# Optimization experiments

Measured on AMD Instinct MI355X. Metric: run time of the kernel, lower is better.

Reference implementation:

```python
import jax, jax.numpy as jnp
import numpy as np

B, L, E, H, D = 2, 2048, 2048, 16, 128
EPS = 1e-6


def _rms(x, scale):
    # RMSNorm over head_dim, computed in float32 (matches torch RMSNorm)
    x32 = x.astype(jnp.float32)
    n = jnp.mean(x32 * x32, axis=-1, keepdims=True)
    return (scale.astype(jnp.float32) * (x32 * jax.lax.rsqrt(n + EPS))).astype(x.dtype)


def _rotary(x, rope):
    # x: [B, L, H, D]; rope: [B, L, D//2, 2]
    xs = x.astype(jnp.float32).reshape(*x.shape[:-1], -1, 2)  # [B,L,H,D/2,2]
    rc = rope.reshape(xs.shape[0], xs.shape[1], 1, xs.shape[3], 2).astype(jnp.float32)
    out = jnp.stack(
        [xs[..., 0] * rc[..., 0] - xs[..., 1] * rc[..., 1],
         xs[..., 1] * rc[..., 0] + xs[..., 0] * rc[..., 1]], -1)
    return out.reshape(x.shape).astype(x.dtype)


def setup_inputs() -> dict:
    key = jax.random.key(0)
    ks = jax.random.split(key, 9)
    s = 0.02  # weight init scale (~kaiming fan_in for E=2048)
    return {
        "inputs_q": jax.random.normal(ks[0], (B, L, E), jnp.float32),
        "inputs_kv": jax.random.normal(ks[1], (B, L, E), jnp.float32),
        "bias": jax.random.normal(ks[2], (B, 1, L, L), jnp.float32),
        "rope_q": jax.random.normal(ks[3], (B, L, D // 2, 2), jnp.float32),
        "rope_k": jax.random.normal(ks[4], (B, L, D // 2, 2), jnp.float32),
        "Wq": jax.random.normal(ks[5], (E, E), jnp.float32) * s,
        "Wk": jax.random.normal(ks[6], (E, E), jnp.float32) * s,
        "Wv": jax.random.normal(ks[7], (E, E), jnp.float32) * s,
        "Wo": jax.random.normal(ks[8], (E, E), jnp.float32) * s,
        "q_scale": jnp.ones((D,), jnp.float32),
        "k_scale": jnp.ones((D,), jnp.float32),
    }


def reference(inputs_q, inputs_kv, bias, rope_q, rope_k, Wq, Wk, Wv, Wo, q_scale, k_scale):
    Bq, Lq, _ = inputs_q.shape
    Lk = inputs_kv.shape[1]
    dtype = inputs_q.dtype
    # QKV projections (torch Linear: y = x @ W.T)
    q = (inputs_q @ Wq.T).reshape(Bq, Lq, H, D)
    k = (inputs_kv @ Wk.T).reshape(Bq, Lk, H, D)
    v = (inputs_kv @ Wv.T).reshape(Bq, Lk, H, D)
    # qk_norm
    q = _rms(q, q_scale)
    k = _rms(k, k_scale)
    # rotary embeddings
    q = _rotary(q, rope_q)
    k = _rotary(k, rope_k)
    # float32_logits
    q = q.astype(jnp.float32)
    k = k.astype(jnp.float32)
    # faithful to torch source: query.div_(depth ** (-0.5)) == q * sqrt(D)
    q = q / (D ** (-0.5))
    logits = jnp.einsum('bqhd,bkhd->bhqk', q, k) + bias.astype(jnp.float32)
    probs = jax.nn.softmax(logits, axis=-1).astype(dtype)
    # dropout_rate = 0.0 -> identity
    x = jnp.einsum('bhqk,bkhd->bqhd', probs, v).reshape(Bq, Lq, E)
    return x @ Wo.T
```

## Files before the change

### kernel.cpp

```cpp
#include <hip/hip_runtime.h>

#define Bb 2
#define Ll 2048
#define Ee 2048
#define Hh 16
#define Dd 128
#define BL (Bb * Ll)
#define NT (Ll / 64)
#define LOSCALE 1024.0f
#define INV_LOSCALE (1.0f / 1024.0f)
#define LOG2E 1.442695041f

typedef float f32x4 __attribute__((ext_vector_type(4)));
typedef _Float16 f16x8 __attribute__((ext_vector_type(8)));

__device__ __forceinline__ void gld_lds16(const void* g, void* l) {
  __builtin_amdgcn_global_load_lds((const __attribute__((address_space(1))) void*)g,
                                   (__attribute__((address_space(3))) void*)l, 16, 0, 0);
}

__device__ __forceinline__ float exp2_hw(float x) {
  float r;
  asm("v_exp_f32 %0, %1" : "=v"(r) : "v"(x));
  return r;
}

__global__ __launch_bounds__(256) void cvt_f32_f16(const float* __restrict__ in,
                                                   _Float16* __restrict__ out, int n4) {
  int i = blockIdx.x * 256 + threadIdx.x;
  if (i < n4) {
    float4 f = ((const float4*)in)[i];
    _Float16 o[4] = {(_Float16)f.x, (_Float16)f.y, (_Float16)f.z, (_Float16)f.w};
    ((uint2*)out)[i] = *(uint2*)o;
  }
}

__global__ __launch_bounds__(256) void cvt_split(const float* __restrict__ in,
                                                 _Float16* __restrict__ hi,
                                                 _Float16* __restrict__ lo, int n4) {
  int i = blockIdx.x * 256 + threadIdx.x;
  if (i < n4) {
    float4 f = ((const float4*)in)[i];
    float fa[4] = {f.x, f.y, f.z, f.w};
    _Float16 h[4], l[4];
    for (int j = 0; j < 4; ++j) {
      h[j] = (_Float16)fa[j];
      l[j] = (_Float16)((fa[j] - (float)h[j]) * LOSCALE);
    }
    ((uint2*)hi)[i] = *(uint2*)h;
    ((uint2*)lo)[i] = *(uint2*)l;
  }
}

__global__ __launch_bounds__(256) void bias_perm(const float* __restrict__ bias,
                                                 _Float16* __restrict__ out) {
  __shared__ float T[128][68];
  const int kt = blockIdx.x, qt = blockIdx.y, b = blockIdx.z;
  const float* src = bias + ((size_t)b * Ll + qt * 128) * Ll + kt * 64;
  const int t = threadIdx.x;
  for (int c = 0; c < 8; ++c) {
    int idx = c * 256 + t;
    int r = idx >> 4, col4 = (idx & 15) * 4;
    float4 v = *(const float4*)&src[(size_t)r * Ll + col4];
    T[r][col4 + 0] = v.x; T[r][col4 + 1] = v.y;
    T[r][col4 + 2] = v.z; T[r][col4 + 3] = v.w;
  }
  __syncthreads();
  _Float16* dst = out + ((((size_t)(b * 8 + (qt >> 1)) * NT + kt) * 16 + (qt & 1) * 8) * 64) * 16;
  for (int s = 0; s < 2; ++s) {
    int slot = t + s * 256;
    int w = slot >> 6, lane = slot & 63;
    int quad = lane >> 4, l16 = lane & 15;
    _Float16 vals[16];
    for (int nt = 0; nt < 4; ++nt)
      for (int r = 0; r < 4; ++r)
        vals[nt * 4 + r] = (_Float16)(T[w * 16 + quad * 4 + r][nt * 16 + l16] * LOG2E);
    *(uint4*)&dst[((size_t)w * 64 + lane) * 16] = *(uint4*)&vals[0];
    *(uint4*)&dst[((size_t)w * 64 + lane) * 16 + 8] = *(uint4*)&vals[8];
  }
}

template <typename OutT>
__global__ __launch_bounds__(256, 2) void gemm_bt(const _Float16* __restrict__ A,
                                                  const _Float16* __restrict__ Bw,
                                                  OutT* __restrict__ C, int M, int N, int K) {
  __shared__ _Float16 As[128 * 64];
  __shared__ _Float16 Bs[128 * 64];
  const int tid = threadIdx.x;
  const int wave = tid >> 6, lane = tid & 63;
  const int quad = lane >> 4, l16 = lane & 15;
  const int lrow = lane >> 3, lch = lane & 7;
  const int scol = (lch ^ lrow) * 8;
  const int bm = blockIdx.y * 128, bn = blockIdx.x * 128;
  const int wm = (wave >> 1) * 64, wn = (wave & 1) * 64;

  f32x4 acc[4][4] = {};

  for (int k0 = 0; k0 < K; k0 += 64) {
    for (int i = 0; i < 4; ++i) {
      int br = wave * 32 + i * 8;
      gld_lds16(&A[(size_t)(bm + br + lrow) * K + k0 + scol], &As[br * 64]);
      gld_lds16(&Bw[(size_t)(bn + br + lrow) * K + k0 + scol], &Bs[br * 64]);
    }
    __syncthreads();
    for (int ks = 0; ks < 2; ++ks) {
      f16x8 af[4], bf[4];
      for (int mt = 0; mt < 4; ++mt)
        af[mt] = *(const f16x8*)&As[(wm + mt * 16 + l16) * 64 +
                                    (((ks * 4 + quad) ^ (l16 & 7)) * 8)];
      for (int nt = 0; nt < 4; ++nt)
        bf[nt] = *(const f16x8*)&Bs[(wn + nt * 16 + l16) * 64 +
                                    (((ks * 4 + quad) ^ (l16 & 7)) * 8)];
      for (int mt = 0; mt < 4; ++mt)
        for (int nt = 0; nt < 4; ++nt)
          acc[mt][nt] = __builtin_amdgcn_mfma_f32_16x16x32_f16(af[mt], bf[nt], acc[mt][nt], 0, 0, 0);
    }
    __syncthreads();
  }

  for (int mt = 0; mt < 4; ++mt)
    for (int nt = 0; nt < 4; ++nt)
      for (int r = 0; r < 4; ++r) {
        int m = bm + wm + mt * 16 + quad * 4 + r;
        int n = bn + wn + nt * 16 + l16;
        C[(size_t)m * N + n] = (OutT)acc[mt][nt][r];
      }
}

__global__ __launch_bounds__(256, 2) void gemm_bt_split(
    const _Float16* __restrict__ Ah, const _Float16* __restrict__ Al,
    const _Float16* __restrict__ Bh, const _Float16* __restrict__ Bl,
    float* __restrict__ C, int M, int N, int K) {
  __shared__ _Float16 Ash[128 * 64];
  __shared__ _Float16 Asl[128 * 64];
  __shared__ _Float16 Bsh[128 * 64];
  __shared__ _Float16 Bsl[128 * 64];
  const int tid = threadIdx.x;
  const int wave = tid >> 6, lane = tid & 63;
  const int quad = lane >> 4, l16 = lane & 15;
  const int lrow = lane >> 3, lch = lane & 7;
  const int scol = (lch ^ lrow) * 8;
  const int bm = blockIdx.y * 128, bn = blockIdx.x * 128;
  const int wm = (wave >> 1) * 64, wn = (wave & 1) * 64;

  f32x4 acc_hh[4][4] = {};
  f32x4 acc_cr[4][4] = {};

  for (int k0 = 0; k0 < K; k0 += 64) {
    for (int i = 0; i < 4; ++i) {
      int br = wave * 32 + i * 8;
      size_t ga = (size_t)(bm + br + lrow) * K + k0 + scol;
      size_t gb = (size_t)(bn + br + lrow) * K + k0 + scol;
      gld_lds16(&Ah[ga], &Ash[br * 64]);
      gld_lds16(&Al[ga], &Asl[br * 64]);
      gld_lds16(&Bh[gb], &Bsh[br * 64]);
      gld_lds16(&Bl[gb], &Bsl[br * 64]);
    }
    __syncthreads();
    for (int ks = 0; ks < 2; ++ks) {
      const int sw = ((ks * 4 + quad) ^ (l16 & 7)) * 8;
      f16x8 afh[4], afl[4], bfh[4], bfl[4];
      for (int mt = 0; mt < 4; ++mt) {
        afh[mt] = *(const f16x8*)&Ash[(wm + mt * 16 + l16) * 64 + sw];
        afl[mt] = *(const f16x8*)&Asl[(wm + mt * 16 + l16) * 64 + sw];
      }
      for (int nt = 0; nt < 4; ++nt) {
        bfh[nt] = *(const f16x8*)&Bsh[(wn + nt * 16 + l16) * 64 + sw];
        bfl[nt] = *(const f16x8*)&Bsl[(wn + nt * 16 + l16) * 64 + sw];
      }
      for (int mt = 0; mt < 4; ++mt)
        for (int nt = 0; nt < 4; ++nt) {
          acc_hh[mt][nt] = __builtin_amdgcn_mfma_f32_16x16x32_f16(afh[mt], bfh[nt], acc_hh[mt][nt], 0, 0, 0);
          acc_cr[mt][nt] = __builtin_amdgcn_mfma_f32_16x16x32_f16(afh[mt], bfl[nt], acc_cr[mt][nt], 0, 0, 0);
          acc_cr[mt][nt] = __builtin_amdgcn_mfma_f32_16x16x32_f16(afl[mt], bfh[nt], acc_cr[mt][nt], 0, 0, 0);
        }
    }
    __syncthreads();
  }

  for (int mt = 0; mt < 4; ++mt)
    for (int nt = 0; nt < 4; ++nt)
      for (int r = 0; r < 4; ++r) {
        int m = bm + wm + mt * 16 + quad * 4 + r;
        int n = bn + wn + nt * 16 + l16;
        C[(size_t)m * N + n] = acc_hh[mt][nt][r] + acc_cr[mt][nt][r] * INV_LOSCALE;
      }
}

__global__ __launch_bounds__(256) void transpose_v(const _Float16* __restrict__ V,
                                                   _Float16* __restrict__ Vt) {
  __shared__ _Float16 T[64][72];
  const int bl0 = blockIdx.x * 64, n0 = blockIdx.y * 64;
  const int tid = threadIdx.x;
  for (int c = 0; c < 2; ++c) {
    int chunk = tid + c * 256;
    int r = chunk >> 3, cc = (chunk & 7) * 8;
    *(uint4*)&T[r][cc] = *(const uint4*)&V[(size_t)(bl0 + r) * Ee + n0 + cc];
  }
  __syncthreads();
  const int b = bl0 >> 11;
  const int k0 = bl0 & (Ll - 1);
  for (int c = 0; c < 2; ++c) {
    int chunk = tid + c * 256;
    int nr = chunk >> 3, kc = (chunk & 7) * 8;
    _Float16 tmp[8];
    for (int j = 0; j < 8; ++j) tmp[j] = T[kc + j][nr];
    *(uint4*)&Vt[((size_t)b * Ee + n0 + nr) * Ll + k0 + kc] = *(uint4*)tmp;
  }
}

__global__ __launch_bounds__(256) void rmsrope(const float* __restrict__ raw,
                                               const float* __restrict__ scale,
                                               const float* __restrict__ rope,
                                               _Float16* __restrict__ outh,
                                               _Float16* __restrict__ outl, float outmul) {
  int row = blockIdx.x * 4 + (threadIdx.x >> 6);
  int t = threadIdx.x & 63;
  float2 x = *(const float2*)&raw[(size_t)row * Dd + 2 * t];
  float ss = x.x * x.x + x.y * x.y;
  for (int off = 1; off < 64; off <<= 1) ss += __shfl_xor(ss, off);
  float inv = rsqrtf(ss * (1.0f / Dd) + 1e-6f);
  float2 sc = *(const float2*)&scale[2 * t];
  float y0 = x.x * inv * sc.x;
  float y1 = x.y * inv * sc.y;
  int bl = row >> 4;
  float2 cs = *(const float2*)&rope[(size_t)bl * Dd + 2 * t];
  float r0 = (y0 * cs.x - y1 * cs.y) * outmul;
  float r1 = (y1 * cs.x + y0 * cs.y) * outmul;
  _Float16 h[2] = {(_Float16)r0, (_Float16)r1};
  _Float16 l[2] = {(_Float16)(r0 - (float)h[0]), (_Float16)(r1 - (float)h[1])};
  *(uint*)&outh[(size_t)row * Dd + 2 * t] = *(uint*)h;
  *(uint*)&outl[(size_t)row * Dd + 2 * t] = *(uint*)l;
}

__global__ __launch_bounds__(512, 2) void attn(const _Float16* __restrict__ Qh_,
                                               const _Float16* __restrict__ Ql_,
                                               const _Float16* __restrict__ Kh_,
                                               const _Float16* __restrict__ Kl_,
                                               const _Float16* __restrict__ Vt_g,
                                               const _Float16* __restrict__ biasp,
                                               _Float16* __restrict__ O) {
  __shared__ _Float16 Ksh[64 * 128];
  __shared__ _Float16 Ksl[64 * 128];
  __shared__ _Float16 Vts[2][128 * 64];
  __shared__ _Float16 Ps[128 * 64];

  const int tid = threadIdx.x;
  const int wave = tid >> 6, lane = tid & 63;
  const int quad = lane >> 4, l16 = lane & 15;
  const int lrow8 = lane >> 3, lch8 = lane & 7;
  const int lrow16 = lane >> 4, lch16 = lane & 15;
  const int h = blockIdx.x;
  const int qt = blockIdx.y, q0 = qt * 128;
  const int b = blockIdx.z;

  f16x8 aqh[4], aql[4];
  {
    size_t qrow = (((size_t)b * Ll + q0 + wave * 16 + l16) * Hh + h) * Dd;
    for (int ks = 0; ks < 4; ++ks) {
      aqh[ks] = *(const f16x8*)&Qh_[qrow + ks * 32 + quad * 8];
      aql[ks] = *(const f16x8*)&Ql_[qrow + ks * 32 + quad * 8];
    }
  }
  const _Float16* Vbase = Vt_g + ((size_t)b * Ee + h * Dd) * Ll;
  const _Float16* bias_base = biasp + (size_t)(b * 8 + (qt >> 1)) * (NT * 16 * 1024) +
                              (size_t)((qt & 1) * 8 + wave) * 1024 + (size_t)lane * 16;

  f32x4 o_acc[8] = {};
  float m_r[4], l_r[4];
  for (int r = 0; r < 4; ++r) { m_r[r] = -1e30f; l_r[r] = 0.f; }

  auto stageK = [&](int kt) {
    const int k0 = kt * 64;
    for (int i = 0; i < 2; ++i) {
      int br = wave * 8 + i * 4;
      int row = br + lrow16;
      int sc = (lch16 ^ (row & 7)) * 8;
      size_t g = (((size_t)b * Ll + k0 + row) * Hh + h) * Dd + sc;
      gld_lds16(&Kh_[g], &Ksh[br * 128]);
      gld_lds16(&Kl_[g], &Ksl[br * 128]);
    }
  };
  auto stageV = [&](int nb, int kt) {
    const int k0 = kt * 64;
    for (int i = 0; i < 2; ++i) {
      int br = wave * 16 + i * 8;
      int row = br + lrow8;
      int sc = (lch8 ^ (row & 7)) * 8;
      gld_lds16(&Vbase[(size_t)row * Ll + k0 + sc], &Vts[nb][br * 64]);
    }
  };

  stageK(0);
  stageV(0, 0);
  __syncthreads();

  for (int kt = 0; kt < NT; ++kt) {
    const int cur = kt & 1;

    f16x8 bf0 = *(const f16x8*)&bias_base[(size_t)kt * 16384];
    f16x8 bf1 = *(const f16x8*)&bias_base[(size_t)kt * 16384 + 8];

    __builtin_amdgcn_s_setprio(1);
    f32x4 s[4] = {};
    for (int ks = 0; ks < 4; ++ks) {
      const int sw = ((ks * 4 + quad) ^ (l16 & 7)) * 8;
      for (int nt = 0; nt < 4; ++nt) {
        f16x8 bkh = *(const f16x8*)&Ksh[(nt * 16 + l16) * 128 + sw];
        f16x8 bkl = *(const f16x8*)&Ksl[(nt * 16 + l16) * 128 + sw];
        s[nt] = __builtin_amdgcn_mfma_f32_16x16x32_f16(aqh[ks], bkh, s[nt], 0, 0, 0);
        s[nt] = __builtin_amdgcn_mfma_f32_16x16x32_f16(aql[ks], bkh, s[nt], 0, 0, 0);
        s[nt] = __builtin_amdgcn_mfma_f32_16x16x32_f16(aqh[ks], bkl, s[nt], 0, 0, 0);
      }
    }
    __builtin_amdgcn_s_setprio(0);

    __syncthreads();

    if (kt + 1 < NT) {
      stageK(kt + 1);
      stageV(cur ^ 1, kt + 1);
    }

#pragma unroll
    for (int nt = 0; nt < 4; ++nt)
#pragma unroll
      for (int r = 0; r < 4; ++r) {
        float bv = (nt < 2) ? (float)bf0[nt * 4 + r] : (float)bf1[nt * 4 + r - 8];
        s[nt][r] += bv;
      }

    bool grow = false;
#pragma unroll
    for (int r = 0; r < 4; ++r) {
      float v = fmaxf(fmaxf(s[0][r], s[1][r]), fmaxf(s[2][r], s[3][r]));
      grow = grow || (v > m_r[r] + 8.f);
    }
    if (__any(grow)) {
#pragma unroll
      for (int r = 0; r < 4; ++r) {
        float v = fmaxf(fmaxf(s[0][r], s[1][r]), fmaxf(s[2][r], s[3][r]));
        for (int off = 1; off < 16; off <<= 1) v = fmaxf(v, __shfl_xor(v, off));
        float mn = fmaxf(m_r[r], v);
        float alpha = exp2_hw(m_r[r] - mn);
        m_r[r] = mn;
        l_r[r] *= alpha;
        for (int ot = 0; ot < 8; ++ot) o_acc[ot][r] *= alpha;
      }
    }
#pragma unroll
    for (int r = 0; r < 4; ++r) {
      int row = wave * 16 + quad * 4 + r;
      float sum = 0.f;
#pragma unroll
      for (int nt = 0; nt < 4; ++nt) {
        float p = exp2_hw(s[nt][r] - m_r[r]);
        sum += p;
        int col = nt * 16 + l16;
        Ps[row * 64 + (col ^ (((row >> 2) & 3) << 4))] = (_Float16)p;
      }
      l_r[r] += sum;
    }

    __builtin_amdgcn_s_setprio(1);
    for (int ks = 0; ks < 2; ++ks) {
      const int sw = ((ks * 4 + quad) ^ (l16 & 7)) * 8;
      int prow = wave * 16 + l16;
      f16x8 ap = *(const f16x8*)&Ps[prow * 64 +
                                    ((ks * 32 + quad * 8) ^ (((l16 >> 2) & 3) << 4))];
      for (int ot = 0; ot < 8; ++ot) {
        f16x8 bv = *(const f16x8*)&Vts[cur][(ot * 16 + l16) * 64 + sw];
        o_acc[ot] = __builtin_amdgcn_mfma_f32_16x16x32_f16(ap, bv, o_acc[ot], 0, 0, 0);
      }
    }
    __builtin_amdgcn_s_setprio(0);

    __syncthreads();
  }

  for (int r = 0; r < 4; ++r) {
    float l = l_r[r];
    for (int off = 1; off < 16; off <<= 1) l += __shfl_xor(l, off);
    l_r[r] = 1.f / l;
  }

  for (int ot = 0; ot < 8; ++ot)
    for (int r = 0; r < 4; ++r) {
      int mm = q0 + wave * 16 + quad * 4 + r;
      O[(((size_t)b * Ll + mm) * Hh + h) * Dd + ot * 16 + l16] =
          (_Float16)(o_acc[ot][r] * l_r[r]);
    }
}

extern "C" void kernel_launch(void* const* d_in, const int* in_sizes, int n_in,
                              void* d_out, int out_size, void* d_ws, size_t ws_size,
                              hipStream_t stream) {
  const float* inputs_q  = (const float*)d_in[0];
  const float* inputs_kv = (const float*)d_in[1];
  const float* bias      = (const float*)d_in[2];
  const float* rope_q    = (const float*)d_in[3];
  const float* rope_k    = (const float*)d_in[4];
  const float* Wq        = (const float*)d_in[5];
  const float* Wk        = (const float*)d_in[6];
  const float* Wv        = (const float*)d_in[7];
  const float* Wo        = (const float*)d_in[8];
  const float* q_scale   = (const float*)d_in[9];
  const float* k_scale   = (const float*)d_in[10];
  float* out = (float*)d_out;

  char* ws = (char*)d_ws;
  size_t o = 0;
  auto alloc = [&](size_t bytes) {
    char* p = ws + o;
    o += (bytes + 255) & ~(size_t)255;
    return p;
  };
  const size_t szX16 = (size_t)BL * Ee * 2;
  const size_t szW16 = (size_t)Ee * Ee * 2;
  _Float16* Xq_hi  = (_Float16*)alloc(szX16);
  _Float16* Xq_lo  = (_Float16*)alloc(szX16);
  _Float16* Xkv_hi = (_Float16*)alloc(szX16);
  _Float16* Xkv_lo = (_Float16*)alloc(szX16);
  _Float16* Wq_hi  = (_Float16*)alloc(szW16);
  _Float16* Wq_lo  = (_Float16*)alloc(szW16);
  _Float16* Wk_hi  = (_Float16*)alloc(szW16);
  _Float16* Wk_lo  = (_Float16*)alloc(szW16);
  _Float16* Wv_hi  = (_Float16*)alloc(szW16);
  _Float16* Wo_hi  = (_Float16*)alloc(szW16);
  float* Qraw = (float*)alloc((size_t)BL * Ee * 4);
  float* Kraw = (float*)alloc((size_t)BL * Ee * 4);
  _Float16* V16 = (_Float16*)alloc(szX16);
  _Float16* Q16h   = Xq_hi;
  _Float16* Q16l   = Xq_lo;
  _Float16* K16h   = Xkv_hi;
  _Float16* K16l   = Xkv_lo;
  _Float16* X16    = (_Float16*)Qraw;
  _Float16* Vt_g   = Wq_hi;
  _Float16* biasp  = (_Float16*)Kraw;

  const int nX4 = BL * Ee / 4;
  const int nW4 = Ee * Ee / 4;
  cvt_split<<<nX4 / 256, 256, 0, stream>>>(inputs_q, Xq_hi, Xq_lo, nX4);
  cvt_split<<<nX4 / 256, 256, 0, stream>>>(inputs_kv, Xkv_hi, Xkv_lo, nX4);
  cvt_split<<<nW4 / 256, 256, 0, stream>>>(Wq, Wq_hi, Wq_lo, nW4);
  cvt_split<<<nW4 / 256, 256, 0, stream>>>(Wk, Wk_hi, Wk_lo, nW4);
  cvt_f32_f16<<<nW4 / 256, 256, 0, stream>>>(Wv, Wv_hi, nW4);
  cvt_f32_f16<<<nW4 / 256, 256, 0, stream>>>(Wo, Wo_hi, nW4);

  dim3 gblk(Ee / 128, BL / 128);
  gemm_bt_split<<<gblk, 256, 0, stream>>>(Xq_hi, Xq_lo, Wq_hi, Wq_lo, Qraw, BL, Ee, Ee);
  gemm_bt_split<<<gblk, 256, 0, stream>>>(Xkv_hi, Xkv_lo, Wk_hi, Wk_lo, Kraw, BL, Ee, Ee);
  gemm_bt<_Float16><<<gblk, 256, 0, stream>>>(Xkv_hi, Wv_hi, V16, BL, Ee, Ee);

  transpose_v<<<dim3(BL / 64, Ee / 64), 256, 0, stream>>>(V16, Vt_g);

  rmsrope<<<BL * Hh / 4, 256, 0, stream>>>(Qraw, q_scale, rope_q, Q16h, Q16l,
                                           sqrtf((float)Dd) * LOG2E);
  rmsrope<<<BL * Hh / 4, 256, 0, stream>>>(Kraw, k_scale, rope_k, K16h, K16l, 1.0f);

  bias_perm<<<dim3(NT, Ll / 128, Bb), 256, 0, stream>>>(bias, biasp);

  attn<<<dim3(Hh, Ll / 128, Bb), 512, 0, stream>>>(Q16h, Q16l, K16h, K16l, Vt_g, biasp, X16);

  gemm_bt<float><<<gblk, 256, 0, stream>>>(X16, Wo_hi, out, BL, Ee, Ee);
}
```

Baseline: 700.4 us.

## Double-buffer K tiles and enlarge attention blocks to 256 query rows

Grows each attention workgroup from 8 to 16 waves, so each block covers 256 query rows and every K/V tile loaded into LDS is shared by twice as many rows. K is now double-buffered like V, and the prefetch of the next tile is issued before the QK MFMAs, which removes one barrier per iteration. The bias indexing is adjusted to match the new tiling. The cost is a 1024-thread block with higher LDS use (K double buffer plus a larger P buffer), which may lower occupancy and halves the number of blocks in the grid.

```diff
diff --git a/kernel.cpp b/kernel.cpp
--- a/kernel.cpp
+++ b/kernel.cpp
@@ -233,17 +233,17 @@
   *(uint*)&outl[(size_t)row * Dd + 2 * t] = *(uint*)l;
 }
 
-__global__ __launch_bounds__(512, 2) void attn(const _Float16* __restrict__ Qh_,
-                                               const _Float16* __restrict__ Ql_,
-                                               const _Float16* __restrict__ Kh_,
-                                               const _Float16* __restrict__ Kl_,
-                                               const _Float16* __restrict__ Vt_g,
-                                               const _Float16* __restrict__ biasp,
-                                               _Float16* __restrict__ O) {
-  __shared__ _Float16 Ksh[64 * 128];
-  __shared__ _Float16 Ksl[64 * 128];
+__global__ __launch_bounds__(1024) void attn(const _Float16* __restrict__ Qh_,
+                                             const _Float16* __restrict__ Ql_,
+                                             const _Float16* __restrict__ Kh_,
+                                             const _Float16* __restrict__ Kl_,
+                                             const _Float16* __restrict__ Vt_g,
+                                             const _Float16* __restrict__ biasp,
+                                             _Float16* __restrict__ O) {
+  __shared__ _Float16 Ksh[2][64 * 128];
+  __shared__ _Float16 Ksl[2][64 * 128];
   __shared__ _Float16 Vts[2][128 * 64];
-  __shared__ _Float16 Ps[128 * 64];
+  __shared__ _Float16 Ps[256 * 64];
 
   const int tid = threadIdx.x;
   const int wave = tid >> 6, lane = tid & 63;
@@ -251,7 +251,7 @@
   const int lrow8 = lane >> 3, lch8 = lane & 7;
   const int lrow16 = lane >> 4, lch16 = lane & 15;
   const int h = blockIdx.x;
-  const int qt = blockIdx.y, q0 = qt * 128;
+  const int qt = blockIdx.y, q0 = qt * 256;
   const int b = blockIdx.z;
 
   f16x8 aqh[4], aql[4];
@@ -263,36 +263,32 @@
     }
   }
   const _Float16* Vbase = Vt_g + ((size_t)b * Ee + h * Dd) * Ll;
-  const _Float16* bias_base = biasp + (size_t)(b * 8 + (qt >> 1)) * (NT * 16 * 1024) +
-                              (size_t)((qt & 1) * 8 + wave) * 1024 + (size_t)lane * 16;
+  const _Float16* bias_base = biasp + (size_t)(b * 8 + qt) * (NT * 16 * 1024) +
+                              (size_t)wave * 1024 + (size_t)lane * 16;
 
   f32x4 o_acc[8] = {};
   float m_r[4], l_r[4];
   for (int r = 0; r < 4; ++r) { m_r[r] = -1e30f; l_r[r] = 0.f; }
 
-  auto stageK = [&](int kt) {
+  auto stage = [&](int nb, int kt) {
     const int k0 = kt * 64;
-    for (int i = 0; i < 2; ++i) {
-      int br = wave * 8 + i * 4;
+    {
+      int br = wave * 4;
       int row = br + lrow16;
       int sc = (lch16 ^ (row & 7)) * 8;
       size_t g = (((size_t)b * Ll + k0 + row) * Hh + h) * Dd + sc;
-      gld_lds16(&Kh_[g], &Ksh[br * 128]);
-      gld_lds16(&Kl_[g], &Ksl[br * 128]);
-    }
-  };
-  auto stageV = [&](int nb, int kt) {
-    const int k0 = kt * 64;
-    for (int i = 0; i < 2; ++i) {
-      int br = wave * 16 + i * 8;
+      gld_lds16(&Kh_[g], &Ksh[nb][br * 128]);
+      gld_lds16(&Kl_[g], &Ksl[nb][br * 128]);
+    }
+    {
+      int br = wave * 8;
       int row = br + lrow8;
       int sc = (lch8 ^ (row & 7)) * 8;
       gld_lds16(&Vbase[(size_t)row * Ll + k0 + sc], &Vts[nb][br * 64]);
     }
   };
 
-  stageK(0);
-  stageV(0, 0);
+  stage(0, 0);
   __syncthreads();
 
   for (int kt = 0; kt < NT; ++kt) {
@@ -300,27 +296,21 @@
 
     f16x8 bf0 = *(const f16x8*)&bias_base[(size_t)kt * 16384];
     f16x8 bf1 = *(const f16x8*)&bias_base[(size_t)kt * 16384 + 8];
+    if (kt + 1 < NT) stage(cur ^ 1, kt + 1);
 
     __builtin_amdgcn_s_setprio(1);
     f32x4 s[4] = {};
     for (int ks = 0; ks < 4; ++ks) {
       const int sw = ((ks * 4 + quad) ^ (l16 & 7)) * 8;
       for (int nt = 0; nt < 4; ++nt) {
-        f16x8 bkh = *(const f16x8*)&Ksh[(nt * 16 + l16) * 128 + sw];
-        f16x8 bkl = *(const f16x8*)&Ksl[(nt * 16 + l16) * 128 + sw];
+        f16x8 bkh = *(const f16x8*)&Ksh[cur][(nt * 16 + l16) * 128 + sw];
+        f16x8 bkl = *(const f16x8*)&Ksl[cur][(nt * 16 + l16) * 128 + sw];
         s[nt] = __builtin_amdgcn_mfma_f32_16x16x32_f16(aqh[ks], bkh, s[nt], 0, 0, 0);
         s[nt] = __builtin_amdgcn_mfma_f32_16x16x32_f16(aql[ks], bkh, s[nt], 0, 0, 0);
         s[nt] = __builtin_amdgcn_mfma_f32_16x16x32_f16(aqh[ks], bkl, s[nt], 0, 0, 0);
       }
     }
     __builtin_amdgcn_s_setprio(0);
-
-    __syncthreads();
-
-    if (kt + 1 < NT) {
-      stageK(kt + 1);
-      stageV(cur ^ 1, kt + 1);
-    }
 
 #pragma unroll
     for (int nt = 0; nt < 4; ++nt)
@@ -374,7 +364,6 @@
       }
     }
     __builtin_amdgcn_s_setprio(0);
-
     __syncthreads();
   }
 
@@ -460,7 +449,7 @@
 
   bias_perm<<<dim3(NT, Ll / 128, Bb), 256, 0, stream>>>(bias, biasp);
 
-  attn<<<dim3(Hh, Ll / 128, Bb), 512, 0, stream>>>(Q16h, Q16l, K16h, K16l, Vt_g, biasp, X16);
+  attn<<<dim3(Hh, Ll / 256, Bb), 1024, 0, stream>>>(Q16h, Q16l, K16h, K16l, Vt_g, biasp, X16);
 
   gemm_bt<float><<<gblk, 256, 0, stream>>>(X16, Wo_hi, out, BL, Ee, Ee);
 }
```

Result: no change. 692.1 us (-1.2%).
